# Kernel tuning notes

Measured on AMD Instinct MI355X. Metric: run time of the kernel, lower is better.

Reference implementation:

```python
import jax, jax.numpy as jnp
import numpy as np

N, E, G = 50000, 800000, 100
H, C = 4, 64


def _gatv2(x, src, dst, ea, Wl, bl, Wr, br, We, att, bias):
    # PyG GATv2Conv: x_l = lin_l(x) (source side), x_r = lin_r(x) (target side)
    xl = (x @ Wl + bl).reshape(-1, H, C)
    xr = (x @ Wr + br).reshape(-1, H, C)
    e = (ea @ We).reshape(-1, H, C)               # [E,H,C]
    m = jax.nn.leaky_relu(xl[src] + xr[dst] + e, negative_slope=0.2)
    alpha = jnp.einsum('ehc,hc->eh', m, att)      # [E,H]
    amax = jax.ops.segment_max(alpha, dst, num_segments=N)
    amax = jnp.where(jnp.isfinite(amax), amax, jnp.float32(0.0))
    ex = jnp.exp(alpha - amax[dst])
    denom = jax.ops.segment_sum(ex, dst, num_segments=N)
    a = ex / (denom[dst] + jnp.float32(1e-16))    # segment softmax over in-edges
    out = jax.ops.segment_sum(xl[src] * a[..., None], dst, num_segments=N)
    return out.reshape(N, H * C) + bias


def setup_inputs() -> dict:
    key = jax.random.key(0)
    ks = jax.random.split(key, 24)
    lin = lambda k, i, o: (jax.random.normal(k, (i, o), jnp.float32) / np.sqrt(i).astype(np.float32))
    x = jax.random.normal(ks[0], (N, 8), jnp.float32)
    edge_index = jnp.stack([jax.random.randint(ks[1], (E,), 0, N),
                            jax.random.randint(ks[2], (E,), 0, N)])
    edge_attr = jax.random.normal(ks[3], (E, 1), jnp.float32)
    batch = jnp.sort(jax.random.randint(ks[4], (N,), 0, G))
    return dict(
        x=x, edge_index=edge_index, edge_attr=edge_attr, batch=batch,
        enc_W=lin(ks[5], 8, 64), enc_b=jnp.zeros((64,), jnp.float32),
        g1_Wl=lin(ks[6], 64, 256), g1_bl=jnp.zeros((256,), jnp.float32),
        g1_Wr=lin(ks[7], 64, 256), g1_br=jnp.zeros((256,), jnp.float32),
        g1_We=lin(ks[8], 1, 256),
        g1_att=jax.random.normal(ks[9], (H, C), jnp.float32) / np.sqrt(C).astype(np.float32),
        g1_bias=jnp.zeros((256,), jnp.float32),
        g2_Wl=lin(ks[10], 256, 256), g2_bl=jnp.zeros((256,), jnp.float32),
        g2_Wr=lin(ks[11], 256, 256), g2_br=jnp.zeros((256,), jnp.float32),
        g2_We=lin(ks[12], 1, 256),
        g2_att=jax.random.normal(ks[13], (H, C), jnp.float32) / np.sqrt(C).astype(np.float32),
        g2_bias=jnp.zeros((256,), jnp.float32),
        p1_W=lin(ks[14], 256, 128), p1_b=jnp.zeros((128,), jnp.float32),
        ln_g=jnp.ones((128,), jnp.float32), ln_b=jnp.zeros((128,), jnp.float32),
        p2_W=lin(ks[15], 128, 64), p2_b=jnp.zeros((64,), jnp.float32),
    )


def reference(x, edge_index, edge_attr, batch,
              enc_W, enc_b,
              g1_Wl, g1_bl, g1_Wr, g1_br, g1_We, g1_att, g1_bias,
              g2_Wl, g2_bl, g2_Wr, g2_br, g2_We, g2_att, g2_bias,
              p1_W, p1_b, ln_g, ln_b, p2_W, p2_b):
    src, dst = edge_index[0], edge_index[1]
    h = jax.nn.relu(x @ enc_W + enc_b)
    h = jax.nn.relu(_gatv2(h, src, dst, edge_attr, g1_Wl, g1_bl, g1_Wr, g1_br, g1_We, g1_att, g1_bias))
    h = jax.nn.relu(_gatv2(h, src, dst, edge_attr, g2_Wl, g2_bl, g2_Wr, g2_br, g2_We, g2_att, g2_bias))
    # global mean pool over graphs
    sums = jax.ops.segment_sum(h, batch, num_segments=G)
    cnt = jax.ops.segment_sum(jnp.ones((N, 1), h.dtype), batch, num_segments=G)
    p = sums / jnp.maximum(cnt, jnp.float32(1.0))
    # post MLP (dropout is identity in eval)
    z = p @ p1_W + p1_b
    mu = jnp.mean(z, axis=-1, keepdims=True)
    var = jnp.mean(jnp.square(z - mu), axis=-1, keepdims=True)
    z = (z - mu) * jax.lax.rsqrt(var + jnp.float32(1e-5)) * ln_g + ln_b
    z = jax.nn.relu(z)
    return jax.nn.relu(z @ p2_W + p2_b)
```

## Files before the change

### kernel.cpp

```cpp
#include <hip/hip_runtime.h>
#include <hip/hip_fp16.h>

#define NH 4
#define CH 64

__global__ void encoder_kernel(const float* __restrict__ x, const float* __restrict__ W,
                               const float* __restrict__ b, float* __restrict__ h, int N) {
  int idx = blockIdx.x * blockDim.x + threadIdx.x;
  if (idx >= N * 64) return;
  int n = idx >> 6, j = idx & 63;
  const float* xp = x + n * 8;
  float acc = b[j];
#pragma unroll
  for (int k = 0; k < 8; ++k) acc = fmaf(xp[k], W[k * 64 + j], acc);
  h[idx] = fmaxf(acc, 0.0f);
}

template <int K>
__global__ void lin_lr_kernel(const float* __restrict__ h,
                              const float* __restrict__ Wl, const float* __restrict__ bl,
                              const float* __restrict__ Wr, const float* __restrict__ br,
                              __half* __restrict__ xl, __half* __restrict__ xr, int N) {
  __shared__ float hs[8][K];
  int n0 = blockIdx.x * 8;
  int j = threadIdx.x;
  int nmax = N - n0; if (nmax > 8) nmax = 8;
  for (int idx = j; idx < nmax * K; idx += 256) {
    int m = idx / K, k = idx % K;
    hs[m][k] = h[(size_t)(n0 + m) * K + k];
  }
  __syncthreads();
  float accl[8], accr[8];
  float bjl = bl[j], bjr = br[j];
#pragma unroll
  for (int m = 0; m < 8; ++m) { accl[m] = bjl; accr[m] = bjr; }
  for (int k = 0; k < K; ++k) {
    float wl = Wl[k * 256 + j];
    float wr = Wr[k * 256 + j];
#pragma unroll
    for (int m = 0; m < 8; ++m) {
      accl[m] = fmaf(hs[m][k], wl, accl[m]);
      accr[m] = fmaf(hs[m][k], wr, accr[m]);
    }
  }
  for (int m = 0; m < nmax; ++m) {
    xl[(size_t)(n0 + m) * 256 + j] = __float2half_rn(accl[m]);
    xr[(size_t)(n0 + m) * 256 + j] = __float2half_rn(accr[m]);
  }
}

__global__ void hist_kernel(const int* __restrict__ dst, int* __restrict__ deg, int E) {
  int e = blockIdx.x * blockDim.x + threadIdx.x;
  if (e < E) atomicAdd(&deg[dst[e]], 1);
}

__global__ void scan_partial_kernel(const int* __restrict__ deg, int* __restrict__ partial, int N) {
  __shared__ int sm[256];
  int t = threadIdx.x;
  int i = blockIdx.x * 256 + t;
  sm[t] = (i < N) ? deg[i] : 0;
  __syncthreads();
#pragma unroll
  for (int s = 128; s > 0; s >>= 1) {
    if (t < s) sm[t] += sm[t + s];
    __syncthreads();
  }
  if (t == 0) partial[blockIdx.x] = sm[0];
}

__global__ void scan_offsets_kernel(int* __restrict__ partial, int nb) {
  __shared__ int sm[256];
  int t = threadIdx.x;
  int v = (t < nb) ? partial[t] : 0;
  sm[t] = v;
  __syncthreads();
#pragma unroll
  for (int off = 1; off < 256; off <<= 1) {
    int a = (t >= off) ? sm[t - off] : 0;
    __syncthreads();
    sm[t] += a;
    __syncthreads();
  }
  if (t < nb) partial[t] = sm[t] - v;
}

__global__ void scan_final_kernel(const int* __restrict__ deg, const int* __restrict__ partial,
                                  int* __restrict__ rowptr, int* __restrict__ cursor, int N, int E) {
  __shared__ int sm[256];
  int t = threadIdx.x;
  int i = blockIdx.x * 256 + t;
  int v = (i < N) ? deg[i] : 0;
  sm[t] = v;
  __syncthreads();
#pragma unroll
  for (int off = 1; off < 256; off <<= 1) {
    int a = (t >= off) ? sm[t - off] : 0;
    __syncthreads();
    sm[t] += a;
    __syncthreads();
  }
  if (i < N) {
    int ex = partial[blockIdx.x] + sm[t] - v;
    rowptr[i] = ex;
    cursor[i] = ex;
  }
  if (i == 0) rowptr[N] = E;
}

__global__ void scatter_build_kernel(const int* __restrict__ src, const int* __restrict__ dst,
                                     const float* __restrict__ ea, int* __restrict__ cursor,
                                     int* __restrict__ srcs, float* __restrict__ eas, int E) {
  int e = blockIdx.x * blockDim.x + threadIdx.x;
  if (e >= E) return;
  int d = dst[e];
  int pos = atomicAdd(&cursor[d], 1);
  srcs[pos] = src[e];
  eas[pos] = ea[e];
}

__device__ __forceinline__ void unpack8(const uint4 r, float o[8]) {
  const __half2* hp = reinterpret_cast<const __half2*>(&r);
#pragma unroll
  for (int k = 0; k < 4; ++k) {
    float2 f = __half22float2(hp[k]);
    o[2 * k] = f.x; o[2 * k + 1] = f.y;
  }
}

__device__ __forceinline__ void pair_accum(const uint4 raw, const float eav, const float mask,
                                           const float xr8[8], const float We8[8], const float at8[8],
                                           float acc[8], float& den) {
  float xlv[8];
  unpack8(raw, xlv);
  float p = 0.f;
#pragma unroll
  for (int c = 0; c < 8; ++c) {
    float v = fmaf(eav, We8[c], xlv[c] + xr8[c]);
    v = (v >= 0.f) ? v : 0.2f * v;
    p = fmaf(v, at8[c], p);
  }
  p += __shfl_xor(p, 1, 64);
  p += __shfl_xor(p, 2, 64);
  p += __shfl_xor(p, 4, 64);
  float ex = __expf(p) * mask;
  den += ex;
#pragma unroll
  for (int c = 0; c < 8; ++c) acc[c] = fmaf(ex, xlv[c], acc[c]);
}

template <bool POOL>
__global__ __launch_bounds__(256)
void gat_aggregate_kernel(const int* __restrict__ rowptr,
                          const int* __restrict__ srcs,
                          const float* __restrict__ eas,
                          const __half* __restrict__ xl,
                          const __half* __restrict__ xr,
                          const float* __restrict__ We,
                          const float* __restrict__ att,
                          const float* __restrict__ bias,
                          float* __restrict__ out,
                          const int* __restrict__ batch,
                          float* __restrict__ sums,
                          float* __restrict__ cnt,
                          int N) {
  int d = (int)((blockIdx.x * (size_t)blockDim.x + threadIdx.x) >> 6);
  int lane = threadIdx.x & 63;
  if (d >= N) return;
  int lq = lane & 31;
  bool lo = (lane < 32);
  const uint4* xlh8 = (const uint4*)xl;
  const uint4* xrh8 = (const uint4*)xr;
  float xr8[8];
  { uint4 r = xrh8[(size_t)d * 32 + lq]; unpack8(r, xr8); }
  float We8[8], at8[8];
#pragma unroll
  for (int k = 0; k < 8; ++k) { We8[k] = We[lq * 8 + k]; at8[k] = att[lq * 8 + k]; }
  int beg = rowptr[d], end = rowptr[d + 1];
  float acc[8];
#pragma unroll
  for (int c = 0; c < 8; ++c) acc[c] = 0.f;
  float den = 0.f;
  int pend = beg + ((end - beg) & ~1);
  int i = beg;
  for (; i + 7 < pend; i += 8) {
    int s0 = srcs[i],     s1 = srcs[i + 1], s2 = srcs[i + 2], s3 = srcs[i + 3];
    int s4 = srcs[i + 4], s5 = srcs[i + 5], s6 = srcs[i + 6], s7 = srcs[i + 7];
    int a0 = lo ? s0 : s1, a1 = lo ? s2 : s3, a2 = lo ? s4 : s5, a3 = lo ? s6 : s7;
    uint4 r0 = xlh8[(size_t)a0 * 32 + lq];
    uint4 r1 = xlh8[(size_t)a1 * 32 + lq];
    uint4 r2 = xlh8[(size_t)a2 * 32 + lq];
    uint4 r3 = xlh8[(size_t)a3 * 32 + lq];
    float e0 = eas[i],     e1 = eas[i + 1], e2 = eas[i + 2], e3 = eas[i + 3];
    float e4 = eas[i + 4], e5 = eas[i + 5], e6 = eas[i + 6], e7 = eas[i + 7];
    float f0 = lo ? e0 : e1, f1 = lo ? e2 : e3, f2 = lo ? e4 : e5, f3 = lo ? e6 : e7;
    pair_accum(r0, f0, 1.f, xr8, We8, at8, acc, den);
    pair_accum(r1, f1, 1.f, xr8, We8, at8, acc, den);
    pair_accum(r2, f2, 1.f, xr8, We8, at8, acc, den);
    pair_accum(r3, f3, 1.f, xr8, We8, at8, acc, den);
  }
  for (; i < pend; i += 2) {
    int s0 = srcs[i], s1 = srcs[i + 1];
    int a0 = lo ? s0 : s1;
    uint4 r0 = xlh8[(size_t)a0 * 32 + lq];
    float f0 = lo ? eas[i] : eas[i + 1];
    pair_accum(r0, f0, 1.f, xr8, We8, at8, acc, den);
  }
  if (pend < end) {
    int s0 = srcs[end - 1];
    uint4 r0 = xlh8[(size_t)s0 * 32 + lq];
    float f0 = eas[end - 1];
    pair_accum(r0, f0, lo ? 1.f : 0.f, xr8, We8, at8, acc, den);
  }
  den += __shfl_xor(den, 32, 64);
#pragma unroll
  for (int c = 0; c < 8; ++c) acc[c] += __shfl_xor(acc[c], 32, 64);
  float inv = 1.f / (den + 1e-16f);
  int half = lane >> 5;
  float c0 = half ? acc[4] : acc[0];
  float c1 = half ? acc[5] : acc[1];
  float c2 = half ? acc[6] : acc[2];
  float c3 = half ? acc[7] : acc[3];
  float4 b4 = ((const float4*)bias)[lq * 2 + half];
  float4 o;
  o.x = fmaxf(fmaf(c0, inv, b4.x), 0.f);
  o.y = fmaxf(fmaf(c1, inv, b4.y), 0.f);
  o.z = fmaxf(fmaf(c2, inv, b4.z), 0.f);
  o.w = fmaxf(fmaf(c3, inv, b4.w), 0.f);
  if (POOL) {
    int g = batch[d];
    float* sg = sums + (size_t)g * 256 + lq * 8 + half * 4;
    atomicAdd(sg + 0, o.x);
    atomicAdd(sg + 1, o.y);
    atomicAdd(sg + 2, o.z);
    atomicAdd(sg + 3, o.w);
    if (lane == 0) atomicAdd(&cnt[g], 1.0f);
  } else {
    ((float4*)out)[(size_t)d * 64 + lq * 2 + half] = o;
  }
}

__global__ void mlp_kernel(const float* __restrict__ sums, const float* __restrict__ cnt,
                           const float* __restrict__ p1W, const float* __restrict__ p1b,
                           const float* __restrict__ lng, const float* __restrict__ lnb,
                           const float* __restrict__ p2W, const float* __restrict__ p2b,
                           float* __restrict__ outp, int G) {
  __shared__ float p[256];
  __shared__ float z[128];
  __shared__ float wsum[2];
  __shared__ float wsum2[2];
  int g = blockIdx.x;
  int t = threadIdx.x;
  float c = fmaxf(cnt[g], 1.0f);
  p[t] = sums[(size_t)g * 256 + t] / c;
  p[t + 128] = sums[(size_t)g * 256 + t + 128] / c;
  __syncthreads();
  float acc = p1b[t];
  for (int k = 0; k < 256; ++k) acc = fmaf(p[k], p1W[k * 128 + t], acc);
  float v = acc;
#pragma unroll
  for (int off = 32; off > 0; off >>= 1) v += __shfl_xor(v, off, 64);
  if ((t & 63) == 0) wsum[t >> 6] = v;
  __syncthreads();
  float mu = (wsum[0] + wsum[1]) * (1.0f / 128.0f);
  float dv = acc - mu;
  float vv = dv * dv;
#pragma unroll
  for (int off = 32; off > 0; off >>= 1) vv += __shfl_xor(vv, off, 64);
  if ((t & 63) == 0) wsum2[t >> 6] = vv;
  __syncthreads();
  float var = (wsum2[0] + wsum2[1]) * (1.0f / 128.0f);
  float zv = dv * rsqrtf(var + 1e-5f) * lng[t] + lnb[t];
  z[t] = fmaxf(zv, 0.0f);
  __syncthreads();
  if (t < 64) {
    float o = p2b[t];
    for (int k = 0; k < 128; ++k) o = fmaf(z[k], p2W[k * 64 + t], o);
    outp[(size_t)g * 64 + t] = fmaxf(o, 0.0f);
  }
}

extern "C" void kernel_launch(void* const* d_in, const int* in_sizes, int n_in,
                              void* d_out, int out_size, void* d_ws, size_t ws_size,
                              hipStream_t stream) {
  const float* x      = (const float*)d_in[0];
  const int*   ei     = (const int*)d_in[1];
  const float* ea     = (const float*)d_in[2];
  const int*   batch  = (const int*)d_in[3];
  const float* enc_W  = (const float*)d_in[4];
  const float* enc_b  = (const float*)d_in[5];
  const float* Wl1    = (const float*)d_in[6];
  const float* bl1    = (const float*)d_in[7];
  const float* Wr1    = (const float*)d_in[8];
  const float* br1    = (const float*)d_in[9];
  const float* We1    = (const float*)d_in[10];
  const float* att1   = (const float*)d_in[11];
  const float* bias1  = (const float*)d_in[12];
  const float* Wl2    = (const float*)d_in[13];
  const float* bl2    = (const float*)d_in[14];
  const float* Wr2    = (const float*)d_in[15];
  const float* br2    = (const float*)d_in[16];
  const float* We2    = (const float*)d_in[17];
  const float* att2   = (const float*)d_in[18];
  const float* bias2  = (const float*)d_in[19];
  const float* p1W    = (const float*)d_in[20];
  const float* p1b    = (const float*)d_in[21];
  const float* lng    = (const float*)d_in[22];
  const float* lnb    = (const float*)d_in[23];
  const float* p2W    = (const float*)d_in[24];
  const float* p2b    = (const float*)d_in[25];
  float* outp = (float*)d_out;

  int N = in_sizes[0] / 8;
  int E = in_sizes[2];
  int G = out_size / 64;
  const int* src = ei;
  const int* dst = ei + E;
  int nb = (N + 255) / 256;

  float* ws      = (float*)d_ws;
  float* h0      = ws;
  __half* xlh    = (__half*)(h0 + (size_t)N * 64);
  __half* xrh    = (__half*)((float*)xlh + (size_t)N * 128);
  float* B2      = (float*)xrh + (size_t)N * 128;
  float* eas     = B2     + (size_t)N * 256;
  float* sums    = eas    + (size_t)E;
  float* cnt     = sums   + (size_t)G * 256;
  int*   srcs    = (int*)(cnt + G);
  int*   rowptr  = srcs + (size_t)E;
  int*   cursor  = rowptr + (size_t)(N + 1);
  int*   partial = cursor + (size_t)N;

  encoder_kernel<<<(N * 64 + 255) / 256, 256, 0, stream>>>(x, enc_W, enc_b, h0, N);

  hipMemsetAsync(cursor, 0, (size_t)N * sizeof(int), stream);
  hist_kernel<<<(E + 255) / 256, 256, 0, stream>>>(dst, cursor, E);
  scan_partial_kernel<<<nb, 256, 0, stream>>>(cursor, partial, N);
  scan_offsets_kernel<<<1, 256, 0, stream>>>(partial, nb);
  scan_final_kernel<<<nb, 256, 0, stream>>>(cursor, partial, rowptr, cursor, N, E);
  scatter_build_kernel<<<(E + 255) / 256, 256, 0, stream>>>(src, dst, ea, cursor, srcs, eas, E);

  lin_lr_kernel<64><<<(N + 7) / 8, 256, 0, stream>>>(h0, Wl1, bl1, Wr1, br1, xlh, xrh, N);
  gat_aggregate_kernel<false><<<(N + 3) / 4, 256, 0, stream>>>(
      rowptr, srcs, eas, xlh, xrh, We1, att1, bias1, B2, nullptr, nullptr, nullptr, N);

  lin_lr_kernel<256><<<(N + 7) / 8, 256, 0, stream>>>(B2, Wl2, bl2, Wr2, br2, xlh, xrh, N);
  hipMemsetAsync(sums, 0, ((size_t)G * 256 + G) * sizeof(float), stream);
  gat_aggregate_kernel<true><<<(N + 3) / 4, 256, 0, stream>>>(
      rowptr, srcs, eas, xlh, xrh, We2, att2, bias2, nullptr, batch, sums, cnt, N);

  mlp_kernel<<<G, 128, 0, stream>>>(sums, cnt, p1W, p1b, lng, lnb, p2W, p2b, outp, G);
}
```

Baseline: 1.072 ms.

## Software-pipeline edge gathers in GAT aggregation with triple-buffered register batches

Replaces the straight unrolled edge loop in the aggregate kernel with a three-stage register pipeline. Batches of four edge pairs are loaded two batches ahead of processing, so gathers of source features stay in flight while earlier batches are accumulated. The intent is to hide gather latency for low-degree nodes (about 16 in-edges on average). In exchange it raises register use (twelve uint4 buffers) and adds per-batch count branches, which may lower occupancy.

```diff
diff --git a/kernel.cpp b/kernel.cpp
--- a/kernel.cpp
+++ b/kernel.cpp
@@ -147,6 +147,35 @@
 #pragma unroll
   for (int c = 0; c < 8; ++c) acc[c] = fmaf(ex, xlv[c], acc[c]);
 }
+
+#define LOADB(R0, R1, R2, R3, F0, F1, F2, F3, kb)                                   \
+  {                                                                                 \
+    int pb_ = (kb) * 4;                                                             \
+    int cnt_ = np - pb_; if (cnt_ > 4) cnt_ = 4;                                    \
+    int ib_ = beg + 2 * pb_;                                                        \
+    if (cnt_ > 0) { int s0_ = srcs[ib_],     s1_ = srcs[ib_ + 1];                   \
+      F0 = lo ? eas[ib_]     : eas[ib_ + 1];                                        \
+      R0 = xlh8[(size_t)(lo ? s0_ : s1_) * 32 + lq]; }                              \
+    if (cnt_ > 1) { int s0_ = srcs[ib_ + 2], s1_ = srcs[ib_ + 3];                   \
+      F1 = lo ? eas[ib_ + 2] : eas[ib_ + 3];                                        \
+      R1 = xlh8[(size_t)(lo ? s0_ : s1_) * 32 + lq]; }                              \
+    if (cnt_ > 2) { int s0_ = srcs[ib_ + 4], s1_ = srcs[ib_ + 5];                   \
+      F2 = lo ? eas[ib_ + 4] : eas[ib_ + 5];                                        \
+      R2 = xlh8[(size_t)(lo ? s0_ : s1_) * 32 + lq]; }                              \
+    if (cnt_ > 3) { int s0_ = srcs[ib_ + 6], s1_ = srcs[ib_ + 7];                   \
+      F3 = lo ? eas[ib_ + 6] : eas[ib_ + 7];                                        \
+      R3 = xlh8[(size_t)(lo ? s0_ : s1_) * 32 + lq]; }                              \
+  }
+
+#define PROCB(R0, R1, R2, R3, F0, F1, F2, F3, kb)                                   \
+  {                                                                                 \
+    int pb_ = (kb) * 4;                                                             \
+    int cnt_ = np - pb_; if (cnt_ > 4) cnt_ = 4;                                    \
+    if (cnt_ > 0) pair_accum(R0, F0, 1.f, xr8, We8, at8, acc, den);                 \
+    if (cnt_ > 1) pair_accum(R1, F1, 1.f, xr8, We8, at8, acc, den);                 \
+    if (cnt_ > 2) pair_accum(R2, F2, 1.f, xr8, We8, at8, acc, den);                 \
+    if (cnt_ > 3) pair_accum(R3, F3, 1.f, xr8, We8, at8, acc, den);                 \
+  }
 
 template <bool POOL>
 __global__ __launch_bounds__(256)
@@ -180,32 +209,27 @@
 #pragma unroll
   for (int c = 0; c < 8; ++c) acc[c] = 0.f;
   float den = 0.f;
-  int pend = beg + ((end - beg) & ~1);
-  int i = beg;
-  for (; i + 7 < pend; i += 8) {
-    int s0 = srcs[i],     s1 = srcs[i + 1], s2 = srcs[i + 2], s3 = srcs[i + 3];
-    int s4 = srcs[i + 4], s5 = srcs[i + 5], s6 = srcs[i + 6], s7 = srcs[i + 7];
-    int a0 = lo ? s0 : s1, a1 = lo ? s2 : s3, a2 = lo ? s4 : s5, a3 = lo ? s6 : s7;
-    uint4 r0 = xlh8[(size_t)a0 * 32 + lq];
-    uint4 r1 = xlh8[(size_t)a1 * 32 + lq];
-    uint4 r2 = xlh8[(size_t)a2 * 32 + lq];
-    uint4 r3 = xlh8[(size_t)a3 * 32 + lq];
-    float e0 = eas[i],     e1 = eas[i + 1], e2 = eas[i + 2], e3 = eas[i + 3];
-    float e4 = eas[i + 4], e5 = eas[i + 5], e6 = eas[i + 6], e7 = eas[i + 7];
-    float f0 = lo ? e0 : e1, f1 = lo ? e2 : e3, f2 = lo ? e4 : e5, f3 = lo ? e6 : e7;
-    pair_accum(r0, f0, 1.f, xr8, We8, at8, acc, den);
-    pair_accum(r1, f1, 1.f, xr8, We8, at8, acc, den);
-    pair_accum(r2, f2, 1.f, xr8, We8, at8, acc, den);
-    pair_accum(r3, f3, 1.f, xr8, We8, at8, acc, den);
-  }
-  for (; i < pend; i += 2) {
-    int s0 = srcs[i], s1 = srcs[i + 1];
-    int a0 = lo ? s0 : s1;
-    uint4 r0 = xlh8[(size_t)a0 * 32 + lq];
-    float f0 = lo ? eas[i] : eas[i + 1];
-    pair_accum(r0, f0, 1.f, xr8, We8, at8, acc, den);
-  }
-  if (pend < end) {
+  int np = (end - beg) >> 1;
+  int nbat = (np + 3) >> 2;
+
+  uint4 a0 = {}, a1 = {}, a2 = {}, a3 = {};
+  uint4 b0 = {}, b1 = {}, b2 = {}, b3 = {};
+  uint4 c0_ = {}, c1_ = {}, c2_ = {}, c3_ = {};
+  float fa0 = 0.f, fa1 = 0.f, fa2 = 0.f, fa3 = 0.f;
+  float fb0 = 0.f, fb1 = 0.f, fb2 = 0.f, fb3 = 0.f;
+  float fc0 = 0.f, fc1 = 0.f, fc2 = 0.f, fc3 = 0.f;
+
+  LOADB(a0, a1, a2, a3, fa0, fa1, fa2, fa3, 0);
+  LOADB(b0, b1, b2, b3, fb0, fb1, fb2, fb3, 1);
+  for (int kb = 0; kb < nbat; kb += 3) {
+    LOADB(c0_, c1_, c2_, c3_, fc0, fc1, fc2, fc3, kb + 2);
+    PROCB(a0, a1, a2, a3, fa0, fa1, fa2, fa3, kb);
+    LOADB(a0, a1, a2, a3, fa0, fa1, fa2, fa3, kb + 3);
+    PROCB(b0, b1, b2, b3, fb0, fb1, fb2, fb3, kb + 1);
+    LOADB(b0, b1, b2, b3, fb0, fb1, fb2, fb3, kb + 4);
+    PROCB(c0_, c1_, c2_, c3_, fc0, fc1, fc2, fc3, kb + 2);
+  }
+  if ((end - beg) & 1) {
     int s0 = srcs[end - 1];
     uint4 r0 = xlh8[(size_t)s0 * 32 + lq];
     float f0 = eas[end - 1];
@@ -216,16 +240,16 @@
   for (int c = 0; c < 8; ++c) acc[c] += __shfl_xor(acc[c], 32, 64);
   float inv = 1.f / (den + 1e-16f);
   int half = lane >> 5;
-  float c0 = half ? acc[4] : acc[0];
-  float c1 = half ? acc[5] : acc[1];
-  float c2 = half ? acc[6] : acc[2];
-  float c3 = half ? acc[7] : acc[3];
+  float o0 = half ? acc[4] : acc[0];
+  float o1 = half ? acc[5] : acc[1];
+  float o2 = half ? acc[6] : acc[2];
+  float o3 = half ? acc[7] : acc[3];
   float4 b4 = ((const float4*)bias)[lq * 2 + half];
   float4 o;
-  o.x = fmaxf(fmaf(c0, inv, b4.x), 0.f);
-  o.y = fmaxf(fmaf(c1, inv, b4.y), 0.f);
-  o.z = fmaxf(fmaf(c2, inv, b4.z), 0.f);
-  o.w = fmaxf(fmaf(c3, inv, b4.w), 0.f);
+  o.x = fmaxf(fmaf(o0, inv, b4.x), 0.f);
+  o.y = fmaxf(fmaf(o1, inv, b4.y), 0.f);
+  o.z = fmaxf(fmaf(o2, inv, b4.z), 0.f);
+  o.w = fmaxf(fmaf(o3, inv, b4.w), 0.f);
   if (POOL) {
     int g = batch[d];
     float* sg = sums + (size_t)g * 256 + lq * 8 + half * 4;
```

Result: slower. 1.145 ms (+6.8%).

## Double-buffer gathered xl rows into LDS via async global_load_lds in aggregation

Applied to the files above, without the earlier changes.

Rewrites the per-destination edge loop of the GAT aggregate kernel to gather source feature rows in chunks of 8 edges directly into per-wave LDS buffers using global_load_lds. Loads for chunk k+1 are issued before chunk k is processed, with explicit vmcnt waits, and source indices are prefetched two chunks ahead. The aim is to hide gather latency behind compute. In exchange it uses 32KB of LDS per block, which may limit occupancy, and it relies on hand-written waitcnt ordering. Average degree is about 16, so the pipeline runs only a few iterations per node.

```diff
diff --git a/kernel.cpp b/kernel.cpp
--- a/kernel.cpp
+++ b/kernel.cpp
@@ -3,6 +3,7 @@
 
 #define NH 4
 #define CH 64
+#define CHUNK 8
 
 __global__ void encoder_kernel(const float* __restrict__ x, const float* __restrict__ W,
                                const float* __restrict__ b, float* __restrict__ h, int N) {
@@ -116,6 +117,12 @@
   int pos = atomicAdd(&cursor[d], 1);
   srcs[pos] = src[e];
   eas[pos] = ea[e];
+}
+
+__device__ __forceinline__ void gload_lds16(const void* g, void* l) {
+  __builtin_amdgcn_global_load_lds(
+      (const __attribute__((address_space(1))) void*)g,
+      (__attribute__((address_space(3))) void*)l, 16, 0, 0);
 }
 
 __device__ __forceinline__ void unpack8(const uint4 r, float o[8]) {
@@ -163,12 +170,14 @@
                           float* __restrict__ sums,
                           float* __restrict__ cnt,
                           int N) {
+  __shared__ __align__(16) char smem[4 * 2 * 4096];
   int d = (int)((blockIdx.x * (size_t)blockDim.x + threadIdx.x) >> 6);
   int lane = threadIdx.x & 63;
   if (d >= N) return;
+  int w = threadIdx.x >> 6;
+  char* mybuf = smem + w * 8192;
   int lq = lane & 31;
   bool lo = (lane < 32);
-  const uint4* xlh8 = (const uint4*)xl;
   const uint4* xrh8 = (const uint4*)xr;
   float xr8[8];
   { uint4 r = xrh8[(size_t)d * 32 + lq]; unpack8(r, xr8); }
@@ -176,56 +185,84 @@
 #pragma unroll
   for (int k = 0; k < 8; ++k) { We8[k] = We[lq * 8 + k]; at8[k] = att[lq * 8 + k]; }
   int beg = rowptr[d], end = rowptr[d + 1];
+  int deg = end - beg;
   float acc[8];
 #pragma unroll
   for (int c = 0; c < 8; ++c) acc[c] = 0.f;
   float den = 0.f;
-  int pend = beg + ((end - beg) & ~1);
-  int i = beg;
-  for (; i + 7 < pend; i += 8) {
-    int s0 = srcs[i],     s1 = srcs[i + 1], s2 = srcs[i + 2], s3 = srcs[i + 3];
-    int s4 = srcs[i + 4], s5 = srcs[i + 5], s6 = srcs[i + 6], s7 = srcs[i + 7];
-    int a0 = lo ? s0 : s1, a1 = lo ? s2 : s3, a2 = lo ? s4 : s5, a3 = lo ? s6 : s7;
-    uint4 r0 = xlh8[(size_t)a0 * 32 + lq];
-    uint4 r1 = xlh8[(size_t)a1 * 32 + lq];
-    uint4 r2 = xlh8[(size_t)a2 * 32 + lq];
-    uint4 r3 = xlh8[(size_t)a3 * 32 + lq];
-    float e0 = eas[i],     e1 = eas[i + 1], e2 = eas[i + 2], e3 = eas[i + 3];
-    float e4 = eas[i + 4], e5 = eas[i + 5], e6 = eas[i + 6], e7 = eas[i + 7];
-    float f0 = lo ? e0 : e1, f1 = lo ? e2 : e3, f2 = lo ? e4 : e5, f3 = lo ? e6 : e7;
-    pair_accum(r0, f0, 1.f, xr8, We8, at8, acc, den);
-    pair_accum(r1, f1, 1.f, xr8, We8, at8, acc, den);
-    pair_accum(r2, f2, 1.f, xr8, We8, at8, acc, den);
-    pair_accum(r3, f3, 1.f, xr8, We8, at8, acc, den);
-  }
-  for (; i < pend; i += 2) {
-    int s0 = srcs[i], s1 = srcs[i + 1];
-    int a0 = lo ? s0 : s1;
-    uint4 r0 = xlh8[(size_t)a0 * 32 + lq];
-    float f0 = lo ? eas[i] : eas[i + 1];
-    pair_accum(r0, f0, 1.f, xr8, We8, at8, acc, den);
-  }
-  if (pend < end) {
-    int s0 = srcs[end - 1];
-    uint4 r0 = xlh8[(size_t)s0 * 32 + lq];
-    float f0 = eas[end - 1];
-    pair_accum(r0, f0, lo ? 1.f : 0.f, xr8, We8, at8, acc, den);
+
+  if (deg > 0) {
+    int nch = (deg + CHUNK - 1) / CHUNK;
+    int dm1 = deg - 1;
+    int s_[8]; float e_[8];
+#pragma unroll
+    for (int j = 0; j < 8; ++j) { int jj = j < dm1 ? j : dm1; s_[j] = srcs[beg + jj]; }
+    {
+      char* b0 = mybuf;
+#pragma unroll
+      for (int p = 0; p < 4; ++p) {
+        int sA = s_[2 * p], sB = s_[2 * p + 1];
+        const char* g = (const char*)xl + (((size_t)(lo ? sA : sB)) << 9) + ((size_t)lq << 4);
+        gload_lds16(g, b0 + p * 1024);
+      }
+    }
+#pragma unroll
+    for (int j = 0; j < 8; ++j) {
+      int j1 = (8 + j) < dm1 ? (8 + j) : dm1;
+      s_[j] = srcs[beg + j1];
+      int j0 = j < dm1 ? j : dm1;
+      e_[j] = eas[beg + j0];
+    }
+    for (int k = 0; k < nch; ++k) {
+      int bufsel = k & 1;
+      if (k + 1 < nch) {
+        char* bn = mybuf + ((k + 1) & 1) * 4096;
+#pragma unroll
+        for (int p = 0; p < 4; ++p) {
+          int sA = s_[2 * p], sB = s_[2 * p + 1];
+          const char* g = (const char*)xl + (((size_t)(lo ? sA : sB)) << 9) + ((size_t)lq << 4);
+          gload_lds16(g, bn + p * 1024);
+        }
+        asm volatile("s_waitcnt vmcnt(4)" ::: "memory");
+      } else {
+        asm volatile("s_waitcnt vmcnt(0)" ::: "memory");
+      }
+      int c = deg - k * CHUNK; if (c > CHUNK) c = CHUNK;
+      int fp = c >> 1, half = c & 1;
+      const char* pb = mybuf + bufsel * 4096;
+#pragma unroll
+      for (int p = 0; p < 4; ++p) {
+        if (p < fp || (p == fp && half)) {
+          uint4 r = *(const uint4*)(pb + p * 1024 + (size_t)lane * 16);
+          float f = lo ? e_[2 * p] : e_[2 * p + 1];
+          float m = (p < fp) ? 1.f : (lo ? 1.f : 0.f);
+          pair_accum(r, f, m, xr8, We8, at8, acc, den);
+        }
+      }
+#pragma unroll
+      for (int j = 0; j < 8; ++j) {
+        int js = (k + 2) * CHUNK + j; js = js < dm1 ? js : dm1;
+        s_[j] = srcs[beg + js];
+        int je = (k + 1) * CHUNK + j; je = je < dm1 ? je : dm1;
+        e_[j] = eas[beg + je];
+      }
+    }
   }
   den += __shfl_xor(den, 32, 64);
 #pragma unroll
   for (int c = 0; c < 8; ++c) acc[c] += __shfl_xor(acc[c], 32, 64);
   float inv = 1.f / (den + 1e-16f);
   int half = lane >> 5;
-  float c0 = half ? acc[4] : acc[0];
-  float c1 = half ? acc[5] : acc[1];
-  float c2 = half ? acc[6] : acc[2];
-  float c3 = half ? acc[7] : acc[3];
+  float o0 = half ? acc[4] : acc[0];
+  float o1 = half ? acc[5] : acc[1];
+  float o2 = half ? acc[6] : acc[2];
+  float o3 = half ? acc[7] : acc[3];
   float4 b4 = ((const float4*)bias)[lq * 2 + half];
   float4 o;
-  o.x = fmaxf(fmaf(c0, inv, b4.x), 0.f);
-  o.y = fmaxf(fmaf(c1, inv, b4.y), 0.f);
-  o.z = fmaxf(fmaf(c2, inv, b4.z), 0.f);
-  o.w = fmaxf(fmaf(c3, inv, b4.w), 0.f);
+  o.x = fmaxf(fmaf(o0, inv, b4.x), 0.f);
+  o.y = fmaxf(fmaf(o1, inv, b4.y), 0.f);
+  o.z = fmaxf(fmaf(o2, inv, b4.z), 0.f);
+  o.w = fmaxf(fmaf(o3, inv, b4.w), 0.f);
   if (POOL) {
     int g = batch[d];
     float* sg = sums + (size_t)g * 256 + lq * 8 + half * 4;
```

New measurement: 1.104 ms. +3.0%, slower.
